# Optimization experiments

Measured on AMD Instinct MI355X. Metric: run time of the kernel, lower is better.

The kernel has to match this reference:

```python
import jax, jax.numpy as jnp
import numpy as np

N = 4096

def setup_inputs() -> dict:
    key = jax.random.key(0)
    k1, k2, k3 = jax.random.split(key, 3)
    x = jax.random.normal(k1, (N, N), dtype=jnp.float32)
    # nn.Linear(N, N, bias=False) weight matrices, shape [out, in] = [N, N]
    s = 1.0 / np.sqrt(N)
    W_r = jax.random.uniform(k2, (N, N), dtype=jnp.float32, minval=-s, maxval=s)
    W_i = jax.random.uniform(k3, (N, N), dtype=jnp.float32, minval=-s, maxval=s)
    return {"x": x, "W_r": W_r, "W_i": W_i}

def reference(x, W_r, W_i):
    # Row pass: fft_in_rows[i] = Linear_real(x[i]) + 1j * Linear_imag(x[i])
    #   => R = x @ W_r^T + 1j * (x @ W_i^T)
    R_r = x @ W_r.T            # [N, N]
    R_i = x @ W_i.T            # [N, N]
    # Column pass: fft_in_cols[:, i] = fft_in_rows[:, i] @ (W_r + 1j W_i)
    #   => C = W^T @ R with W = W_r + 1j W_i (complex matmul in real arithmetic)
    C_r = W_r.T @ R_r - W_i.T @ R_i
    C_i = W_r.T @ R_i + W_i.T @ R_r
    # res = cat([real, imag], dim=1) -> [N, 2N]
    return jnp.concatenate([C_r, C_i], axis=1)
```

## Files before the change

kernel.cpp:

```cpp
#include <hip/hip_runtime.h>
#include <hip/hip_bf16.h>

#define NN 4096

typedef unsigned short u16;
using bf16x8 = __attribute__((ext_vector_type(8))) short;
using f32x4  = __attribute__((ext_vector_type(4))) float;
using u32x4  = __attribute__((ext_vector_type(4))) unsigned int;

__device__ inline u16 f2bf(float f) {
    union { float f; unsigned u; } c; c.f = f;
    unsigned r = (c.u + 0x7fffu + ((c.u >> 16) & 1u)) >> 16;
    return (u16)r;
}

__device__ inline void gld16(const void* g, void* l) {
    __builtin_amdgcn_global_load_lds(
        (const __attribute__((address_space(1))) void*)g,
        (__attribute__((address_space(3))) void*)l, 16, 0, 0);
}

__device__ inline bf16x8 negbf(bf16x8 v) {
    u32x4 u; __builtin_memcpy(&u, &v, 16);
    u ^= 0x80008000u;
    bf16x8 r; __builtin_memcpy(&r, &u, 16);
    return r;
}

__global__ __launch_bounds__(256) void cvt_bf16(const float* __restrict__ s,
                                                u16* __restrict__ d) {
    size_t i = ((size_t)blockIdx.x * 256 + threadIdx.x) * 8;
    float4 v0 = *(const float4*)(s + i);
    float4 v1 = *(const float4*)(s + i + 4);
    bf16x8 o;
    o[0] = (short)f2bf(v0.x); o[1] = (short)f2bf(v0.y);
    o[2] = (short)f2bf(v0.z); o[3] = (short)f2bf(v0.w);
    o[4] = (short)f2bf(v1.x); o[5] = (short)f2bf(v1.y);
    o[6] = (short)f2bf(v1.z); o[7] = (short)f2bf(v1.w);
    *(bf16x8*)(d + i) = o;
}

__global__ __launch_bounds__(256) void tr_cvt(const float* __restrict__ s,
                                              u16* __restrict__ d) {
    __shared__ float t[32][33];
    int x  = blockIdx.x * 32 + threadIdx.x;
    int y0 = blockIdx.y * 32;
#pragma unroll
    for (int j = 0; j < 32; j += 8)
        t[threadIdx.y + j][threadIdx.x] = s[(size_t)(y0 + threadIdx.y + j) * NN + x];
    __syncthreads();
    int x2 = blockIdx.y * 32 + threadIdx.x;
    int y2 = blockIdx.x * 32;
#pragma unroll
    for (int j = 0; j < 32; j += 8)
        d[(size_t)(y2 + threadIdx.y + j) * NN + x2] = f2bf(t[threadIdx.x][threadIdx.y + j]);
}


__global__ __launch_bounds__(256) void gemm_nt_dual(
    const u16* __restrict__ A0, const u16* __restrict__ A1,
    const u16* __restrict__ B,
    u16* __restrict__ C0, u16* __restrict__ C1) {
    __shared__ u16 sm[2][2][4096];
    const u16* A = blockIdx.z ? A1 : A0;
    u16*       C = blockIdx.z ? C1 : C0;

    const int tid  = threadIdx.x;
    const int lane = tid & 63;
    const int wid  = tid >> 6;
    const int wm   = (wid >> 1) * 64;
    const int wn   = (wid & 1) * 64;
    const int brow = blockIdx.y * 128;
    const int bcol = blockIdx.x * 128;

    f32x4 acc[4][4] = {};

    const int r0 = tid >> 2;
    const int lb = (tid & 3) ^ ((r0 >> 1) & 3);
    const size_t aoff0 = (size_t)(brow + r0) * NN + lb * 8;
    const size_t aoff1 = aoff0 + (size_t)64 * NN;
    const size_t boff0 = (size_t)(bcol + r0) * NN + lb * 8;
    const size_t boff1 = boff0 + (size_t)64 * NN;
    const int rl = lane & 15;
    const int kg = (((lane >> 4) ^ ((rl >> 1) & 3))) * 8;

#define STAGE1(buf, kk) do { \
    gld16(A + aoff0 + (kk), &sm[buf][0][tid * 8]); \
    gld16(A + aoff1 + (kk), &sm[buf][0][2048 + tid * 8]); \
    gld16(B + boff0 + (kk), &sm[buf][1][tid * 8]); \
    gld16(B + boff1 + (kk), &sm[buf][1][2048 + tid * 8]); \
} while (0)

    auto compute = [&](int buf) {
        bf16x8 a[4], b[4];
#pragma unroll
        for (int i = 0; i < 4; i++)
            a[i] = *(const bf16x8*)&sm[buf][0][(wm + i * 16 + rl) * 32 + kg];
#pragma unroll
        for (int j = 0; j < 4; j++)
            b[j] = *(const bf16x8*)&sm[buf][1][(wn + j * 16 + rl) * 32 + kg];
#pragma unroll
        for (int i = 0; i < 4; i++)
#pragma unroll
            for (int j = 0; j < 4; j++)
                acc[i][j] = __builtin_amdgcn_mfma_f32_16x16x32_bf16(a[i], b[j], acc[i][j], 0, 0, 0);
    };

    STAGE1(0, 0);
    __syncthreads();
    int cur = 0;
    for (int t = 0; t < NN / 32 - 1; t++) {
        STAGE1(cur ^ 1, (t + 1) * 32);
        compute(cur);
        __syncthreads();
        cur ^= 1;
    }
    compute(cur);

    const int rg = (lane >> 4) * 4;
#pragma unroll
    for (int i = 0; i < 4; i++)
#pragma unroll
        for (int j = 0; j < 4; j++) {
            int col = bcol + wn + j * 16 + (lane & 15);
#pragma unroll
            for (int r = 0; r < 4; r++) {
                int row = brow + wm + i * 16 + rg + r;
                C[(size_t)row * NN + col] = f2bf(acc[i][j][r]);
            }
        }
#undef STAGE1
}

__global__ __launch_bounds__(256, 2) void gemm_pass2(
    const u16* __restrict__ Ar, const u16* __restrict__ Ai,
    const u16* __restrict__ Br, const u16* __restrict__ Bi,
    float* __restrict__ Out) {
    __shared__ u16 sm[2][4][4096];

    const int tid  = threadIdx.x;
    const int lane = tid & 63;
    const int wid  = tid >> 6;
    const int wm   = (wid >> 1) * 64;
    const int wn   = (wid & 1) * 64;
    const int brow = blockIdx.y * 128;
    const int bcol = blockIdx.x * 128;

    f32x4 accr[4][4] = {};
    f32x4 acci[4][4] = {};

    const int r0 = tid >> 2;
    const int lb = (tid & 3) ^ ((r0 >> 1) & 3);
    const size_t moff0 = (size_t)(brow + r0) * NN + lb * 8;
    const size_t moff1 = moff0 + (size_t)64 * NN;
    const size_t noff0 = (size_t)(bcol + r0) * NN + lb * 8;
    const size_t noff1 = noff0 + (size_t)64 * NN;
    const int rl = lane & 15;
    const int kg = (((lane >> 4) ^ ((rl >> 1) & 3))) * 8;

#define STAGE2(buf, kk) do { \
    gld16(Ar + moff0 + (kk), &sm[buf][0][tid * 8]); \
    gld16(Ar + moff1 + (kk), &sm[buf][0][2048 + tid * 8]); \
    gld16(Ai + moff0 + (kk), &sm[buf][1][tid * 8]); \
    gld16(Ai + moff1 + (kk), &sm[buf][1][2048 + tid * 8]); \
    gld16(Br + noff0 + (kk), &sm[buf][2][tid * 8]); \
    gld16(Br + noff1 + (kk), &sm[buf][2][2048 + tid * 8]); \
    gld16(Bi + noff0 + (kk), &sm[buf][3][tid * 8]); \
    gld16(Bi + noff1 + (kk), &sm[buf][3][2048 + tid * 8]); \
} while (0)

    auto compute = [&](int buf) {
        bf16x8 ar[4], ai[4], br[4], bi[4];
#pragma unroll
        for (int i = 0; i < 4; i++) {
            ar[i] = *(const bf16x8*)&sm[buf][0][(wm + i * 16 + rl) * 32 + kg];
            ai[i] = *(const bf16x8*)&sm[buf][1][(wm + i * 16 + rl) * 32 + kg];
        }
#pragma unroll
        for (int j = 0; j < 4; j++) {
            br[j] = *(const bf16x8*)&sm[buf][2][(wn + j * 16 + rl) * 32 + kg];
            bi[j] = *(const bf16x8*)&sm[buf][3][(wn + j * 16 + rl) * 32 + kg];
        }
#pragma unroll
        for (int i = 0; i < 4; i++)
#pragma unroll
            for (int j = 0; j < 4; j++) {
                acci[i][j] = __builtin_amdgcn_mfma_f32_16x16x32_bf16(ar[i], bi[j], acci[i][j], 0, 0, 0);
                acci[i][j] = __builtin_amdgcn_mfma_f32_16x16x32_bf16(ai[i], br[j], acci[i][j], 0, 0, 0);
            }
#pragma unroll
        for (int i = 0; i < 4; i++) ai[i] = negbf(ai[i]);
#pragma unroll
        for (int i = 0; i < 4; i++)
#pragma unroll
            for (int j = 0; j < 4; j++) {
                accr[i][j] = __builtin_amdgcn_mfma_f32_16x16x32_bf16(ar[i], br[j], accr[i][j], 0, 0, 0);
                accr[i][j] = __builtin_amdgcn_mfma_f32_16x16x32_bf16(ai[i], bi[j], accr[i][j], 0, 0, 0);
            }
    };

    STAGE2(0, 0);
    __syncthreads();
    int cur = 0;
    for (int t = 0; t < NN / 32 - 1; t++) {
        STAGE2(cur ^ 1, (t + 1) * 32);
        compute(cur);
        __syncthreads();
        cur ^= 1;
    }
    compute(cur);

    const int rg = (lane >> 4) * 4;
#pragma unroll
    for (int i = 0; i < 4; i++)
#pragma unroll
        for (int j = 0; j < 4; j++) {
            int col = bcol + wn + j * 16 + (lane & 15);
#pragma unroll
            for (int r = 0; r < 4; r++) {
                int row = brow + wm + i * 16 + rg + r;
                Out[(size_t)row * (2 * NN) + col]      = accr[i][j][r];
                Out[(size_t)row * (2 * NN) + NN + col] = acci[i][j][r];
            }
        }
#undef STAGE2
}

extern "C" void kernel_launch(void* const* d_in, const int* in_sizes, int n_in,
                              void* d_out, int out_size, void* d_ws, size_t ws_size,
                              hipStream_t stream) {
    const float* x  = (const float*)d_in[0];
    const float* Wr = (const float*)d_in[1];
    const float* Wi = (const float*)d_in[2];
    float* out = (float*)d_out;

    const size_t SZ = (size_t)NN * NN;
    u16* ws  = (u16*)d_ws;
    u16* xb  = ws;
    u16* Wrb = ws + SZ;
    u16* Wib = ws + 2 * SZ;
    u16* Rtr = ws + 3 * SZ;
    u16* Rti = ws + 4 * SZ;

    cvt_bf16<<<8192, 256, 0, stream>>>(x,  xb);
    cvt_bf16<<<8192, 256, 0, stream>>>(Wr, Wrb);
    cvt_bf16<<<8192, 256, 0, stream>>>(Wi, Wib);

    gemm_nt_dual<<<dim3(32, 32, 2), 256, 0, stream>>>(Wrb, Wib, xb, Rtr, Rti);

    u16* WrT = xb;
    u16* WiT = Wrb;
    tr_cvt<<<dim3(128, 128), dim3(32, 8), 0, stream>>>(Wr, WrT);
    tr_cvt<<<dim3(128, 128), dim3(32, 8), 0, stream>>>(Wi, WiT);

    gemm_pass2<<<dim3(32, 32), 256, 0, stream>>>(WrT, WiT, Rtr, Rti, out);
}
```

Measured before the change: 870.5 us.

## Fuse pass-1 dual GEMMs sharing B tile and add XCD-aware tile swizzle

Result: faster. 786.5 us (-9.7%).

```diff
diff --git a/kernel.cpp b/kernel.cpp
--- a/kernel.cpp
+++ b/kernel.cpp
@@ -25,6 +25,15 @@
     u ^= 0x80008000u;
     bf16x8 r; __builtin_memcpy(&r, &u, 16);
     return r;
+}
+
+__device__ inline void swz_tile(int bid, int& brow, int& bcol) {
+    const int xcd   = bid & 7;
+    const int local = bid >> 3;
+    const int rr    = xcd >> 1;
+    const int rc    = xcd & 1;
+    brow = (rr * 8  + (local >> 4)) * 128;
+    bcol = (rc * 16 + (local & 15)) * 128;
 }
 
 __global__ __launch_bounds__(256) void cvt_bf16(const float* __restrict__ s,
@@ -57,23 +66,23 @@
 }
 
 
-__global__ __launch_bounds__(256) void gemm_nt_dual(
-    const u16* __restrict__ A0, const u16* __restrict__ A1,
+__global__ __launch_bounds__(256, 2) void gemm_pass1(
+    const u16* __restrict__ Ar, const u16* __restrict__ Ai,
     const u16* __restrict__ B,
-    u16* __restrict__ C0, u16* __restrict__ C1) {
-    __shared__ u16 sm[2][2][4096];
-    const u16* A = blockIdx.z ? A1 : A0;
-    u16*       C = blockIdx.z ? C1 : C0;
+    u16* __restrict__ Cr, u16* __restrict__ Ci) {
+    __shared__ u16 sm[2][3][4096];
+
+    int brow, bcol;
+    swz_tile(blockIdx.x, brow, bcol);
 
     const int tid  = threadIdx.x;
     const int lane = tid & 63;
     const int wid  = tid >> 6;
     const int wm   = (wid >> 1) * 64;
     const int wn   = (wid & 1) * 64;
-    const int brow = blockIdx.y * 128;
-    const int bcol = blockIdx.x * 128;
-
-    f32x4 acc[4][4] = {};
+
+    f32x4 accr[4][4] = {};
+    f32x4 acci[4][4] = {};
 
     const int r0 = tid >> 2;
     const int lb = (tid & 3) ^ ((r0 >> 1) & 3);
@@ -82,35 +91,41 @@
     const size_t boff0 = (size_t)(bcol + r0) * NN + lb * 8;
     const size_t boff1 = boff0 + (size_t)64 * NN;
     const int rl = lane & 15;
-    const int kg = (((lane >> 4) ^ ((rl >> 1) & 3))) * 8;
-
-#define STAGE1(buf, kk) do { \
-    gld16(A + aoff0 + (kk), &sm[buf][0][tid * 8]); \
-    gld16(A + aoff1 + (kk), &sm[buf][0][2048 + tid * 8]); \
-    gld16(B + boff0 + (kk), &sm[buf][1][tid * 8]); \
-    gld16(B + boff1 + (kk), &sm[buf][1][2048 + tid * 8]); \
+    const int kg = ((lane >> 4) ^ ((rl >> 1) & 3)) * 8;
+
+#define STG1(buf, kk) do { \
+    gld16(Ar + aoff0 + (kk), &sm[buf][0][tid * 8]); \
+    gld16(Ar + aoff1 + (kk), &sm[buf][0][2048 + tid * 8]); \
+    gld16(Ai + aoff0 + (kk), &sm[buf][1][tid * 8]); \
+    gld16(Ai + aoff1 + (kk), &sm[buf][1][2048 + tid * 8]); \
+    gld16(B  + boff0 + (kk), &sm[buf][2][tid * 8]); \
+    gld16(B  + boff1 + (kk), &sm[buf][2][2048 + tid * 8]); \
 } while (0)
 
     auto compute = [&](int buf) {
-        bf16x8 a[4], b[4];
+        bf16x8 ar[4], ai[4], b[4];
+#pragma unroll
+        for (int i = 0; i < 4; i++) {
+            ar[i] = *(const bf16x8*)&sm[buf][0][(wm + i * 16 + rl) * 32 + kg];
+            ai[i] = *(const bf16x8*)&sm[buf][1][(wm + i * 16 + rl) * 32 + kg];
+        }
+#pragma unroll
+        for (int j = 0; j < 4; j++)
+            b[j] = *(const bf16x8*)&sm[buf][2][(wn + j * 16 + rl) * 32 + kg];
 #pragma unroll
         for (int i = 0; i < 4; i++)
-            a[i] = *(const bf16x8*)&sm[buf][0][(wm + i * 16 + rl) * 32 + kg];
-#pragma unroll
-        for (int j = 0; j < 4; j++)
-            b[j] = *(const bf16x8*)&sm[buf][1][(wn + j * 16 + rl) * 32 + kg];
-#pragma unroll
-        for (int i = 0; i < 4; i++)
-#pragma unroll
-            for (int j = 0; j < 4; j++)
-                acc[i][j] = __builtin_amdgcn_mfma_f32_16x16x32_bf16(a[i], b[j], acc[i][j], 0, 0, 0);
+#pragma unroll
+            for (int j = 0; j < 4; j++) {
+                accr[i][j] = __builtin_amdgcn_mfma_f32_16x16x32_bf16(ar[i], b[j], accr[i][j], 0, 0, 0);
+                acci[i][j] = __builtin_amdgcn_mfma_f32_16x16x32_bf16(ai[i], b[j], acci[i][j], 0, 0, 0);
+            }
     };
 
-    STAGE1(0, 0);
+    STG1(0, 0);
     __syncthreads();
     int cur = 0;
     for (int t = 0; t < NN / 32 - 1; t++) {
-        STAGE1(cur ^ 1, (t + 1) * 32);
+        STG1(cur ^ 1, (t + 1) * 32);
         compute(cur);
         __syncthreads();
         cur ^= 1;
@@ -122,14 +137,15 @@
     for (int i = 0; i < 4; i++)
 #pragma unroll
         for (int j = 0; j < 4; j++) {
-            int col = bcol + wn + j * 16 + (lane & 15);
+            int col = bcol + wn + j * 16 + rl;
 #pragma unroll
             for (int r = 0; r < 4; r++) {
                 int row = brow + wm + i * 16 + rg + r;
-                C[(size_t)row * NN + col] = f2bf(acc[i][j][r]);
-            }
-        }
-#undef STAGE1
+                Cr[(size_t)row * NN + col] = f2bf(accr[i][j][r]);
+                Ci[(size_t)row * NN + col] = f2bf(acci[i][j][r]);
+            }
+        }
+#undef STG1
 }
 
 __global__ __launch_bounds__(256, 2) void gemm_pass2(
@@ -138,13 +154,14 @@
     float* __restrict__ Out) {
     __shared__ u16 sm[2][4][4096];
 
+    int brow, bcol;
+    swz_tile(blockIdx.x, brow, bcol);
+
     const int tid  = threadIdx.x;
     const int lane = tid & 63;
     const int wid  = tid >> 6;
     const int wm   = (wid >> 1) * 64;
     const int wn   = (wid & 1) * 64;
-    const int brow = blockIdx.y * 128;
-    const int bcol = blockIdx.x * 128;
 
     f32x4 accr[4][4] = {};
     f32x4 acci[4][4] = {};
@@ -156,7 +173,7 @@
     const size_t noff0 = (size_t)(bcol + r0) * NN + lb * 8;
     const size_t noff1 = noff0 + (size_t)64 * NN;
     const int rl = lane & 15;
-    const int kg = (((lane >> 4) ^ ((rl >> 1) & 3))) * 8;
+    const int kg = ((lane >> 4) ^ ((rl >> 1) & 3)) * 8;
 
 #define STAGE2(buf, kk) do { \
     gld16(Ar + moff0 + (kk), &sm[buf][0][tid * 8]); \
@@ -215,7 +232,7 @@
     for (int i = 0; i < 4; i++)
 #pragma unroll
         for (int j = 0; j < 4; j++) {
-            int col = bcol + wn + j * 16 + (lane & 15);
+            int col = bcol + wn + j * 16 + rl;
 #pragma unroll
             for (int r = 0; r < 4; r++) {
                 int row = brow + wm + i * 16 + rg + r;
@@ -246,12 +263,12 @@
     cvt_bf16<<<8192, 256, 0, stream>>>(Wr, Wrb);
     cvt_bf16<<<8192, 256, 0, stream>>>(Wi, Wib);
 
-    gemm_nt_dual<<<dim3(32, 32, 2), 256, 0, stream>>>(Wrb, Wib, xb, Rtr, Rti);
+    gemm_pass1<<<1024, 256, 0, stream>>>(Wrb, Wib, xb, Rtr, Rti);
 
     u16* WrT = xb;
     u16* WiT = Wrb;
     tr_cvt<<<dim3(128, 128), dim3(32, 8), 0, stream>>>(Wr, WrT);
     tr_cvt<<<dim3(128, 128), dim3(32, 8), 0, stream>>>(Wi, WiT);
 
-    gemm_pass2<<<dim3(32, 32), 256, 0, stream>>>(WrT, WiT, Rtr, Rti, out);
-}
+    gemm_pass2<<<1024, 256, 0, stream>>>(WrT, WiT, Rtr, Rti, out);
+}
```
